# Performance work log

Measured on AMD Instinct MI355X. Metric: run time of the kernel, lower is better.

## Reference

```python
import math
import jax, jax.numpy as jnp
import numpy as np

B, N, D = 16, 2048, 256
EPS = 1e-8  # torch cosine_similarity default eps
TAU = 3.0   # gumbel-softmax temperature


def setup_inputs() -> dict:
    key = jax.random.key(0)
    k1, k2 = jax.random.split(key)
    return {
        "LowLevelFeatures": jax.random.normal(k1, (B, 1, N, D), dtype=jnp.float32),
        "HighLevelFeatures": jax.random.normal(k2, (B, 1, N, D), dtype=jnp.float32),
        "batch_size": B,
    }


def _forward(LLF4, HLF4):
    LLF = LLF4[:, 0]  # [B,N,D]
    HLF = HLF4[:, 0]  # [B,N,D]
    b, n, d = LLF.shape
    # pairwise cosine similarity [B,N,N]: matmul + norm-product (same math as
    # torch's broadcast cosine_similarity, without the [B,N,N,D] intermediate)
    dots = jnp.einsum('bnd,bmd->bnm', LLF, HLF)
    nl = jnp.linalg.norm(LLF, axis=-1)  # [B,N]
    nh = jnp.linalg.norm(HLF, axis=-1)  # [B,N]
    sim = dots / jnp.maximum(nl[:, :, None] * nh[:, None, :], EPS)
    sim = sim / math.sqrt(d)
    probs = jax.nn.softmax(sim, axis=1)  # softmax over dim 1 (LLF rows)
    # F.gumbel_softmax(probs, tau=3, hard=True, dim=1): probs act as logits
    u = jax.random.uniform(jax.random.key(42), probs.shape,
                           minval=1e-10, maxval=1.0)
    gumbels = -jnp.log(-jnp.log(u))
    y_soft = jax.nn.softmax((probs + gumbels) / TAU, axis=1)
    idx = jnp.argmax(y_soft, axis=1)  # [B,N]: selected LLF-row n per HLF col m
    # torch.where on the one-hot scans row-major over (b, n, m), so per batch
    # the returned n-indices are the SORTED multiset of selected indices
    sl = jnp.sort(idx, axis=-1)  # [B,N]
    bidx = jnp.arange(b)[:, None]  # [B,1]
    aligned = HLF[bidx, sl]  # gather along dim 1 -> [B,N,D]
    # rowwise cosine similarity between gathered HLF and LLF
    w = jnp.sum(aligned * LLF, axis=-1) / jnp.maximum(
        jnp.linalg.norm(aligned, axis=-1) * nl, EPS)  # [B,N]
    noise = jax.nn.softmax(w / 0.1, axis=1)[:, :, None]  # [B,N,1]
    hlf_new = aligned + LLF * noise
    out = HLF.at[bidx, sl].set(hlf_new)
    return out


def reference(LowLevelFeatures, HighLevelFeatures, batch_size):
    return _forward(LowLevelFeatures, HighLevelFeatures)
```

## Files before the change

kernel.cpp:

```cpp
#include <hip/hip_runtime.h>
#include <math.h>

#define NB 16
#define NN 2048
#define ND 256
#define BNtot (NB*NN)
#define HH 33554432u

typedef __attribute__((ext_vector_type(8))) short bf16x8;
typedef __attribute__((ext_vector_type(4))) float f32x4;

__device__ __forceinline__ void gld16(const void* g, void* l){
  __builtin_amdgcn_global_load_lds((const __attribute__((address_space(1))) void*)g,
                                   (__attribute__((address_space(3))) void*)l, 16, 0, 0);
}

__device__ __forceinline__ unsigned rotl(unsigned v, int r){
  return __builtin_amdgcn_alignbit(v, v, 32-r);
}
__device__ __forceinline__ unsigned umaxu(unsigned a, unsigned b){ return a > b ? a : b; }
__device__ __forceinline__ unsigned uminu(unsigned a, unsigned b){ return a < b ? a : b; }

__device__ __forceinline__ float gumbelv(unsigned b, unsigned n, unsigned m){
  unsigned f = (b<<22) | (n<<11) | m;
  unsigned x0 = (b < 8u) ? f : (f - HH);
  unsigned x1 = x0 + HH;
  const unsigned ks0=0u, ks1=42u, ks2=0u^42u^0x1BD11BDAu;
  unsigned v0 = x0 + ks0;
  unsigned v1 = x1 + ks1;
#define TFR(r) { v0 += v1; v1 = rotl(v1,(r)); v1 ^= v0; }
  TFR(13) TFR(15) TFR(26) TFR(6)
  v0 += ks1; v1 += ks2 + 1u;
  TFR(17) TFR(29) TFR(16) TFR(24)
  v0 += ks2; v1 += ks0 + 2u;
  TFR(13) TFR(15) TFR(26) TFR(6)
  v0 += ks0; v1 += ks1 + 3u;
  TFR(17) TFR(29) TFR(16) TFR(24)
  v0 += ks1; v1 += ks2 + 4u;
  TFR(13) TFR(15) TFR(26) TFR(6)
  v0 += ks2; v1 += ks0 + 5u;
#undef TFR
  unsigned bits = (b < 8u) ? v0 : v1;
  float fl = __uint_as_float((bits>>9) | 0x3F800000u) - 1.0f;
  float u = fmaxf(1e-10f, fl + 1e-10f);
  return -logf(-logf(u));
}

__device__ __forceinline__ float gfromkey(unsigned key){
  float fl = __uint_as_float(key | 0x3F800000u) - 1.0f;
  float u = fmaxf(1e-10f, fl + 1e-10f);
  return -logf(-logf(u));
}

struct GumState {
  unsigned x0, vk, a1, a2, c1, c2;
  int t;
};

__device__ __forceinline__ void gum_init(GumState& g, int t){
  g.t = t;
  int half = t & 1;
  int m    = (t >> 1) & 2047;
  int bl   = (t >> 12) & 7;
  int nq   = t >> 15;
  int nstart = (nq << 7) + (half << 6);
  g.x0 = ((unsigned)bl << 22) | ((unsigned)nstart << 11) | (unsigned)m;
  g.a1 = g.a2 = g.c1 = g.c2 = 0;
  g.vk = (unsigned)(127 - (half<<6));
}

__device__ __forceinline__ void gum_seek(GumState& g, int o){
  g.x0 += (unsigned)o * 2048u;
  g.vk -= (unsigned)o;
}

__device__ __forceinline__ void gum_iter(GumState& g, const int cnt){
  const unsigned KS2 = 42u ^ 0x1BD11BDAu;
  unsigned x0=g.x0, vk=g.vk, a1=g.a1, a2=g.a2, c1=g.c1, c2=g.c2;
#define TFR(r)       { v0 += v1; v1 = rotl(v1,(r)); v1 ^= v0; }
#define TFRI(r, inj) { v0 += v1 + (inj); v1 = rotl(v1,(r)); v1 ^= v0; }
  #pragma unroll 4
  for (int j = 0; j < cnt; ++j){
    unsigned v0 = x0;
    unsigned v1 = x0 + (HH + 42u);
    TFR(13) TFR(15) TFR(26) TFR(6)
    v1 += KS2 + 1u;
    TFRI(17, 42u) TFR(29) TFR(16) TFR(24)
    v1 += 2u;
    TFRI(13, KS2) TFR(15) TFR(26) TFR(6)
    v1 += 42u + 3u;
    TFR(17) TFR(29) TFR(16) TFR(24)
    v1 += KS2 + 4u;
    TFRI(13, 42u) TFR(15) TFR(26) TFR(6)
    v0 += KS2; v1 += 5u;
    unsigned pa = (v0 & 0xFFFFFE00u) | vk;
    unsigned pb = (v1 & 0xFFFFFE00u) | vk;
    unsigned ta = uminu(pa, a1);
    a1 = umaxu(pa, a1);
    a2 = umaxu(ta, a2);
    unsigned tc = uminu(pb, c1);
    c1 = umaxu(pb, c1);
    c2 = umaxu(tc, c2);
    x0 += 2048u;
    vk -= 1u;
  }
#undef TFR
#undef TFRI
  g.x0=x0; g.vk=vk; g.a1=a1; g.a2=a2; g.c1=c1; g.c2=c2;
}

__device__ __forceinline__ void gum_finish(const GumState& g, unsigned* __restrict__ pck,
                                           int seg){
  int half = g.t & 1;
  int m    = (g.t >> 1) & 2047;
  int bl   = (g.t >> 12) & 7;
  int nq   = g.t >> 15;
  unsigned p1 = __shfl_xor((int)g.a1, 1), p2 = __shfl_xor((int)g.a2, 1);
  unsigned q1 = __shfl_xor((int)g.c1, 1), q2 = __shfl_xor((int)g.c2, 1);
  unsigned A1 = umaxu(g.a1, p1);
  unsigned A2 = umaxu(uminu(g.a1, p1), umaxu(g.a2, p2));
  unsigned C1 = umaxu(g.c1, q1);
  unsigned C2 = umaxu(uminu(g.c1, q1), umaxu(g.c2, q2));
  if (half == 0){
    size_t base = ((size_t)((nq<<2) + (seg<<1))*NB + bl)*NN + m;
    pck[base]                 = A1;
    pck[base + (size_t)BNtot] = A2;
    pck[base + 8*NN]                 = C1;
    pck[base + 8*NN + (size_t)BNtot] = C2;
  }
}

__launch_bounds__(256)
__global__ void kgumbel(unsigned* __restrict__ pck){
  GumState g; gum_init(g, blockIdx.x*256 + (int)threadIdx.x);
  gum_iter(g, 32);
  gum_finish(g, pck, 0);
  g.a1 = g.a2 = g.c1 = g.c2 = 0;
  gum_iter(g, 32);
  gum_finish(g, pck, 1);
}

__device__ __forceinline__ void prep_rows(const float4* v, int wid, int lane,
                                          ushort* __restrict__ dst, float* __restrict__ nrm){
  #pragma unroll
  for (int i=0;i<4;i++){
    int row = wid*4 + i;
    float s = v[i].x*v[i].x + v[i].y*v[i].y + v[i].z*v[i].z + v[i].w*v[i].w;
    for (int o=32;o;o>>=1) s += __shfl_down(s,o);
    if (lane==0) nrm[row] = sqrtf(s);
    uint2 u;
    u.x = (__float_as_uint(v[i].y)&0xFFFF0000u)|(__float_as_uint(v[i].x)>>16);
    u.y = (__float_as_uint(v[i].w)&0xFFFF0000u)|(__float_as_uint(v[i].z)>>16);
    int b = row >> 11, nloc = row & 2047;
    int k = lane << 2;
    int ck = k >> 6;
    int j  = k & 63;
    int qi = j >> 3;
    size_t off = (size_t)b*524288 + (size_t)ck*131072 + (size_t)nloc*64
               + ((qi ^ (nloc & 7)) << 3) + (j & 7);
    *(uint2*)(dst + off) = u;
  }
}

__global__ void knorms(const float* __restrict__ LLF, const float* __restrict__ HLF,
                       float* __restrict__ nl, float* __restrict__ nh){
  int row = blockIdx.x;
  int wave = threadIdx.x >> 6;
  int lane = threadIdx.x & 63;
  const float* src = wave ? HLF : LLF;
  float4 v = ((const float4*)(src + (size_t)row*ND))[lane];
  float s = v.x*v.x + v.y*v.y + v.z*v.z + v.w*v.w;
  for (int o=32;o;o>>=1) s += __shfl_down(s,o);
  if (lane==0) (wave? nh: nl)[row] = sqrtf(s);
}

__launch_bounds__(256, 8)
__global__ void kfuse1(const float* __restrict__ LLF, const float* __restrict__ HLF,
                       ushort* __restrict__ Abf, ushort* __restrict__ Bbf,
                       float* __restrict__ nl, float* __restrict__ nh,
                       unsigned* __restrict__ pck){
  int t = blockIdx.x*256 + (int)threadIdx.x;
  int wid = t >> 6;
  int lane = t & 63;
  GumState g; gum_init(g, t);
  float4 va[4];
  #pragma unroll
  for (int i=0;i<4;i++)
    va[i] = ((const float4*)(LLF + (size_t)(wid*4+i)*ND))[lane];
  gum_iter(g, 16);
  prep_rows(va, wid, lane, Abf, nl);
  float4 vb[4];
  #pragma unroll
  for (int i=0;i<4;i++)
    vb[i] = ((const float4*)(HLF + (size_t)(wid*4+i)*ND))[lane];
  gum_iter(g, 16);
  prep_rows(vb, wid, lane, Bbf, nh);
  gum_finish(g, pck, 0);
}

#define K1 0.09016844f
__launch_bounds__(256)
__global__ void kgemm_dma(const ushort* __restrict__ Abf, const ushort* __restrict__ Bbf,
                          const float* __restrict__ nl, const float* __restrict__ nh,
                          float* __restrict__ partS, unsigned* __restrict__ pck){
  __shared__ ushort As[128*64];
  __shared__ ushort Bs[128*64];
  __shared__ float colsum[128];
  const int b  = blockIdx.z;
  const int n0 = blockIdx.y << 7;
  const int m0 = blockIdx.x << 7;
  const int tid  = threadIdx.x;
  const int lane = tid & 63;
  const int w    = tid >> 6;
  const int wn   = w >> 1, wm = w & 1;
  const int quad = lane >> 4, l15 = lane & 15;
  if (tid < 128) colsum[tid] = 0.0f;

  const int blockflat = (blockIdx.z*16 + (int)blockIdx.y)*16 + (int)blockIdx.x;
  const bool gw = (w < 2);
  GumState gs;
  if (gw){
    gum_init(gs, (blockflat*2 + w)*64 + lane);
    gum_seek(gs, 32);
  }

  const ushort* Ab = Abf + (size_t)b*524288;
  const ushort* Bb = Bbf + (size_t)b*524288;

  f32x4 acc[4][4];
  #pragma unroll
  for (int i=0;i<4;i++)
    #pragma unroll
    for (int j=0;j<4;j++) acc[i][j] = (f32x4){0.f,0.f,0.f,0.f};

  for (int ck=0; ck<4; ck++){
    __syncthreads();
    const ushort* ga = Ab + (size_t)ck*131072 + (size_t)n0*64;
    const ushort* gb = Bb + (size_t)ck*131072 + (size_t)m0*64;
    #pragma unroll
    for (int t=0;t<4;t++){
      int seg = (w*4 + t) * 512;
      gld16(ga + seg + lane*8, &As[seg]);
      gld16(gb + seg + lane*8, &Bs[seg]);
    }
    if (gw) gum_iter(gs, 8);
    __syncthreads();
    #pragma unroll
    for (int ks=0; ks<64; ks+=32){
      bf16x8 af[4], bf[4];
      #pragma unroll
      for (int t=0;t<4;t++){
        int R = wn*64 + t*16 + l15;
        af[t] = *(const bf16x8*)(&As[R*64 + ((((ks>>3)+quad) ^ (R&7))<<3)]);
      }
      #pragma unroll
      for (int t=0;t<4;t++){
        int R = wm*64 + t*16 + l15;
        bf[t] = *(const bf16x8*)(&Bs[R*64 + ((((ks>>3)+quad) ^ (R&7))<<3)]);
      }
      #pragma unroll
      for (int ti=0;ti<4;ti++)
        #pragma unroll
        for (int tj=0;tj<4;tj++)
          acc[ti][tj] = __builtin_amdgcn_mfma_f32_16x16x32_bf16(af[ti], bf[tj], acc[ti][tj], 0, 0, 0);
    }
  }

  float an[4][4];
  #pragma unroll
  for (int ti=0;ti<4;ti++)
    #pragma unroll
    for (int r=0;r<4;r++)
      an[ti][r] = K1 / nl[b*NN + n0 + wn*64 + ti*16 + quad*4 + r];
  float bm[4];
  #pragma unroll
  for (int tj=0;tj<4;tj++)
    bm[tj] = 1.0f / nh[b*NN + m0 + wm*64 + tj*16 + l15];
  #pragma unroll
  for (int tj=0;tj<4;tj++){
    float s = 0.0f;
    #pragma unroll
    for (int ti=0;ti<4;ti++)
      #pragma unroll
      for (int r=0;r<4;r++)
        s += __builtin_amdgcn_exp2f(acc[ti][tj][r]*an[ti][r]*bm[tj] - K1);
    s += __shfl_down(s, 32);
    s += __shfl_down(s, 16);
    if (lane < 16) atomicAdd(&colsum[wm*64 + tj*16 + l15], s);
  }
  __syncthreads();
  if (tid < 128)
    partS[(size_t)blockIdx.y*BNtot + b*NN + m0 + tid] = colsum[tid];
  if (gw) gum_finish(gs, pck, 1);
}

__launch_bounds__(256)
__global__ void kgemm_mfma(const float* __restrict__ LLF, const float* __restrict__ HLF,
                           const float* __restrict__ nl, const float* __restrict__ nh,
                           float* __restrict__ partS){
  __shared__ ushort As[128][72];
  __shared__ ushort Bs[128][72];
  __shared__ float colsum[128];
  const int b  = blockIdx.z;
  const int n0 = blockIdx.y << 7;
  const int m0 = blockIdx.x << 7;
  const float* Ab = LLF + (size_t)b*NN*ND;
  const float* Bb = HLF + (size_t)b*NN*ND;
  const int tid  = threadIdx.x;
  const int lane = tid & 63;
  const int w    = tid >> 6;
  const int wn   = w >> 1, wm = w & 1;
  const int quad = lane >> 4, l15 = lane & 15;
  if (tid < 128) colsum[tid] = 0.0f;

  f32x4 acc[4][4];
  #pragma unroll
  for (int i=0;i<4;i++)
    #pragma unroll
    for (int j=0;j<4;j++) acc[i][j] = (f32x4){0.f,0.f,0.f,0.f};

  const int rbase = tid >> 3;
  const int kq    = (tid & 7) << 3;

  for (int ck=0; ck<4; ck++){
    const int k0 = ck << 6;
    __syncthreads();
    #pragma unroll
    for (int pi=0; pi<4; pi++){
      int row = rbase + (pi<<5);
      const float* pa = Ab + (size_t)(n0+row)*ND + k0 + kq;
      float4 a0 = *(const float4*)pa;
      float4 a1 = *(const float4*)(pa+4);
      uint4 ua;
      ua.x = (__float_as_uint(a0.y)&0xFFFF0000u)|(__float_as_uint(a0.x)>>16);
      ua.y = (__float_as_uint(a0.w)&0xFFFF0000u)|(__float_as_uint(a0.z)>>16);
      ua.z = (__float_as_uint(a1.y)&0xFFFF0000u)|(__float_as_uint(a1.x)>>16);
      ua.w = (__float_as_uint(a1.w)&0xFFFF0000u)|(__float_as_uint(a1.z)>>16);
      *(uint4*)(&As[row][kq]) = ua;
      const float* pb = Bb + (size_t)(m0+row)*ND + k0 + kq;
      float4 b0 = *(const float4*)pb;
      float4 b1 = *(const float4*)(pb+4);
      uint4 ub;
      ub.x = (__float_as_uint(b0.y)&0xFFFF0000u)|(__float_as_uint(b0.x)>>16);
      ub.y = (__float_as_uint(b0.w)&0xFFFF0000u)|(__float_as_uint(b0.z)>>16);
      ub.z = (__float_as_uint(b1.y)&0xFFFF0000u)|(__float_as_uint(b1.x)>>16);
      ub.w = (__float_as_uint(b1.w)&0xFFFF0000u)|(__float_as_uint(b1.z)>>16);
      *(uint4*)(&Bs[row][kq]) = ub;
    }
    __syncthreads();
    #pragma unroll
    for (int ks=0; ks<64; ks+=32){
      bf16x8 af[4], bf[4];
      #pragma unroll
      for (int t=0;t<4;t++)
        af[t] = *(const bf16x8*)(&As[wn*64 + t*16 + l15][ks + quad*8]);
      #pragma unroll
      for (int t=0;t<4;t++)
        bf[t] = *(const bf16x8*)(&Bs[wm*64 + t*16 + l15][ks + quad*8]);
      #pragma unroll
      for (int ti=0;ti<4;ti++)
        #pragma unroll
        for (int tj=0;tj<4;tj++)
          acc[ti][tj] = __builtin_amdgcn_mfma_f32_16x16x32_bf16(af[ti], bf[tj], acc[ti][tj], 0, 0, 0);
    }
  }

  float an[4][4];
  #pragma unroll
  for (int ti=0;ti<4;ti++)
    #pragma unroll
    for (int r=0;r<4;r++)
      an[ti][r] = K1 / nl[b*NN + n0 + wn*64 + ti*16 + quad*4 + r];
  float bm[4];
  #pragma unroll
  for (int tj=0;tj<4;tj++)
    bm[tj] = 1.0f / nh[b*NN + m0 + wm*64 + tj*16 + l15];
  #pragma unroll
  for (int tj=0;tj<4;tj++){
    float s = 0.0f;
    #pragma unroll
    for (int ti=0;ti<4;ti++)
      #pragma unroll
      for (int r=0;r<4;r++)
        s += __builtin_amdgcn_exp2f(acc[ti][tj][r]*an[ti][r]*bm[tj] - K1);
    s += __shfl_down(s, 32);
    s += __shfl_down(s, 16);
    if (lane < 16) atomicAdd(&colsum[wm*64 + tj*16 + l15], s);
  }
  __syncthreads();
  if (tid < 128)
    partS[(size_t)blockIdx.y*BNtot + b*NN + m0 + tid] = colsum[tid];
}

__launch_bounds__(256)
__global__ void kresolve(const float* __restrict__ LLF, const float* __restrict__ HLF,
                         const float* __restrict__ nl, const float* __restrict__ nh,
                         const float* __restrict__ partS,
                         const unsigned* __restrict__ pck,
                         int* __restrict__ idx){
  int w    = threadIdx.x >> 6;
  int lane = threadIdx.x & 63;
  int g = blockIdx.x*4 + w;
  int b = g >> 11;
  float ps = (lane < 16) ? partS[(size_t)lane*BNtot + g] : 0.0f;
  ps += __shfl_down(ps, 8);
  ps += __shfl_down(ps, 4);
  ps += __shfl_down(ps, 2);
  ps += __shfl_down(ps, 1);
  float invS = 1.0f / __shfl(ps, 0);
  unsigned pk = pck[(size_t)lane*BNtot + g];
  float pv = gfromkey(pk >> 9);
  int   pn = ((lane >> 2) << 7) + 127 - (int)(pk & 127u);
  float gmax = pv;
  for (int o=32;o;o>>=1) gmax = fmaxf(gmax, __shfl_down(gmax,o));
  gmax = __shfl(gmax, 0);
  unsigned long long mask = __ballot(pv >= gmax - 8e-5f);
  float4 h = ((const float4*)(HLF + (size_t)g*ND))[lane];
  float nhg = nh[g];
  float bestQ = -INFINITY; int bestN = 1<<30;
  while (mask){
    int src = __builtin_ctzll(mask); mask &= mask-1;
    int   n  = __shfl(pn, src);
    float gv = __shfl(pv, src);
    float4 a = ((const float4*)(LLF + ((size_t)b*NN + n)*ND))[lane];
    float d = a.x*h.x + a.y*h.y + a.z*h.z + a.w*h.w;
    for (int o=32;o;o>>=1) d += __shfl_down(d,o);
    d = __shfl(d, 0);
    float sim = (d / fmaxf(nl[b*NN+n]*nhg, 1e-8f)) * 0.0625f;
    float q = expf(sim - 0.0625f)*invS + gv;
    if (q > bestQ || (q == bestQ && n < bestN)){ bestQ = q; bestN = n; }
  }
  if (lane==0) idx[g] = bestN;
}

__launch_bounds__(256)
__global__ void kstats(const float* __restrict__ A, const float* __restrict__ Bm,
                       const float* __restrict__ nl, const float* __restrict__ nh,
                       float* __restrict__ Mout, float* __restrict__ Sinv){
  __shared__ float As[64][33];
  __shared__ float Bs[64][33];
  __shared__ float Cs[64][65];
  const int b  = blockIdx.x >> 5;
  const int m0 = (blockIdx.x & 31) << 6;
  const float* Ab = A  + (size_t)b*NN*ND;
  const float* Bb = Bm + (size_t)b*NN*ND;
  const int tid = threadIdx.x;
  const int tx = tid & 15, ty = tid >> 4;
  float nhv[4];
  #pragma unroll
  for (int j=0;j<4;j++) nhv[j] = nh[b*NN + m0 + tx*4 + j];
  float Mr = -INFINITY, Sr = 0.0f;
  for (int nt=0; nt<NN; nt+=64){
    float acc[4][4] = {{0.f,0.f,0.f,0.f},{0.f,0.f,0.f,0.f},{0.f,0.f,0.f,0.f},{0.f,0.f,0.f,0.f}};
    for (int kc=0; kc<ND; kc+=32){
      __syncthreads();
      #pragma unroll
      for (int s=0;s<2;s++){
        int f = tid + (s<<8);
        int r = f >> 3;
        int c = (f & 7) << 2;
        float4 va = *(const float4*)(Ab + (size_t)(nt+r)*ND + kc + c);
        As[r][c]=va.x; As[r][c+1]=va.y; As[r][c+2]=va.z; As[r][c+3]=va.w;
        float4 vb = *(const float4*)(Bb + (size_t)(m0+r)*ND + kc + c);
        Bs[r][c]=vb.x; Bs[r][c+1]=vb.y; Bs[r][c+2]=vb.z; Bs[r][c+3]=vb.w;
      }
      __syncthreads();
      #pragma unroll 4
      for (int k=0;k<32;k++){
        float a0=As[ty*4+0][k], a1=As[ty*4+1][k], a2=As[ty*4+2][k], a3=As[ty*4+3][k];
        float b0=Bs[tx*4+0][k], b1=Bs[tx*4+1][k], b2=Bs[tx*4+2][k], b3=Bs[tx*4+3][k];
        acc[0][0]+=a0*b0; acc[0][1]+=a0*b1; acc[0][2]+=a0*b2; acc[0][3]+=a0*b3;
        acc[1][0]+=a1*b0; acc[1][1]+=a1*b1; acc[1][2]+=a1*b2; acc[1][3]+=a1*b3;
        acc[2][0]+=a2*b0; acc[2][1]+=a2*b1; acc[2][2]+=a2*b2; acc[2][3]+=a2*b3;
        acc[3][0]+=a3*b0; acc[3][1]+=a3*b1; acc[3][2]+=a3*b2; acc[3][3]+=a3*b3;
      }
    }
    float nlv[4];
    #pragma unroll
    for (int i=0;i<4;i++) nlv[i] = nl[b*NN + nt + ty*4 + i];
    __syncthreads();
    #pragma unroll
    for (int i=0;i<4;i++)
      #pragma unroll
      for (int j=0;j<4;j++){
        float denom = fmaxf(nlv[i]*nhv[j], 1e-8f);
        Cs[ty*4+i][tx*4+j] = (acc[i][j]/denom)*0.0625f;
      }
    __syncthreads();
    if (tid < 64){
      float tmax = -INFINITY;
      #pragma unroll 8
      for (int r=0;r<64;r++) tmax = fmaxf(tmax, Cs[r][tid]);
      float newM = fmaxf(Mr, tmax);
      float s = 0.0f;
      #pragma unroll 4
      for (int r=0;r<64;r++) s += expf(Cs[r][tid]-newM);
      Sr = Sr*expf(Mr-newM) + s;
      Mr = newM;
    }
  }
  if (tid < 64){
    Mout[b*NN+m0+tid] = Mr;
    Sinv[b*NN+m0+tid] = 1.0f/Sr;
  }
}

__launch_bounds__(256)
__global__ void kargmax(const float* __restrict__ A, const float* __restrict__ Bm,
                        const float* __restrict__ nl, const float* __restrict__ nh,
                        const float* __restrict__ Mv, const float* __restrict__ Sv,
                        int* __restrict__ idxout){
  __shared__ float As[64][33];
  __shared__ float Bs[64][33];
  __shared__ float Vs[16][64];
  __shared__ int   Is[16][64];
  const int b  = blockIdx.x >> 5;
  const int m0 = (blockIdx.x & 31) << 6;
  const float* Ab = A  + (size_t)b*NN*ND;
  const float* Bb = Bm + (size_t)b*NN*ND;
  const int tid = threadIdx.x;
  const int tx = tid & 15, ty = tid >> 4;
  float nhv[4], Mj[4], iSj[4];
  #pragma unroll
  for (int j=0;j<4;j++){
    int m = m0 + tx*4 + j;
    nhv[j] = nh[b*NN + m];
    Mj[j]  = Mv[b*NN + m];
    iSj[j] = Sv[b*NN + m];
  }
  float bestV = -INFINITY; int bestN = 0;
  for (int nt=0; nt<NN; nt+=64){
    float acc[4][4] = {{0.f,0.f,0.f,0.f},{0.f,0.f,0.f,0.f},{0.f,0.f,0.f,0.f},{0.f,0.f,0.f,0.f}};
    for (int kc=0; kc<ND; kc+=32){
      __syncthreads();
      #pragma unroll
      for (int s=0;s<2;s++){
        int f = tid + (s<<8);
        int r = f >> 3;
        int c = (f & 7) << 2;
        float4 va = *(const float4*)(Ab + (size_t)(nt+r)*ND + kc + c);
        As[r][c]=va.x; As[r][c+1]=va.y; As[r][c+2]=va.z; As[r][c+3]=va.w;
        float4 vb = *(const float4*)(Bb + (size_t)(m0+r)*ND + kc + c);
        Bs[r][c]=vb.x; Bs[r][c+1]=vb.y; Bs[r][c+2]=vb.z; Bs[r][c+3]=vb.w;
      }
      __syncthreads();
      #pragma unroll 4
      for (int k=0;k<32;k++){
        float a0=As[ty*4+0][k], a1=As[ty*4+1][k], a2=As[ty*4+2][k], a3=As[ty*4+3][k];
        float b0=Bs[tx*4+0][k], b1=Bs[tx*4+1][k], b2=Bs[tx*4+2][k], b3=Bs[tx*4+3][k];
        acc[0][0]+=a0*b0; acc[0][1]+=a0*b1; acc[0][2]+=a0*b2; acc[0][3]+=a0*b3;
        acc[1][0]+=a1*b0; acc[1][1]+=a1*b1; acc[1][2]+=a1*b2; acc[1][3]+=a1*b3;
        acc[2][0]+=a2*b0; acc[2][1]+=a2*b1; acc[2][2]+=a2*b2; acc[2][3]+=a2*b3;
        acc[3][0]+=a3*b0; acc[3][1]+=a3*b1; acc[3][2]+=a3*b2; acc[3][3]+=a3*b3;
      }
    }
    float nlv[4];
    #pragma unroll
    for (int i=0;i<4;i++) nlv[i] = nl[b*NN + nt + ty*4 + i];
    float lv[4]; int li[4];
    #pragma unroll
    for (int j=0;j<4;j++){ lv[j] = -INFINITY; li[j] = 0; }
    #pragma unroll
    for (int i=0;i<4;i++){
      int n = nt + ty*4 + i;
      #pragma unroll
      for (int j=0;j<4;j++){
        float denom = fmaxf(nlv[i]*nhv[j], 1e-8f);
        float sim = (acc[i][j]/denom)*0.0625f;
        float p = expf(sim - Mj[j]) * iSj[j];
        float v = p + gumbelv((unsigned)b, (unsigned)n, (unsigned)(m0 + tx*4 + j));
        if (v > lv[j]) { lv[j] = v; li[j] = n; }
      }
    }
    __syncthreads();
    #pragma unroll
    for (int j=0;j<4;j++){ Vs[ty][tx*4+j]=lv[j]; Is[ty][tx*4+j]=li[j]; }
    __syncthreads();
    if (tid < 64){
      #pragma unroll 4
      for (int t=0;t<16;t++){
        float v = Vs[t][tid];
        if (v > bestV){ bestV = v; bestN = Is[t][tid]; }
      }
    }
  }
  if (tid < 64) idxout[b*NN + m0 + tid] = bestN;
}

__global__ void ksort(const int* __restrict__ idx, int* __restrict__ cntg,
                      int* __restrict__ offg, int* __restrict__ sl){
  __shared__ int c[NN];
  __shared__ int part[256];
  int b = blockIdx.x, tid = threadIdx.x;
  for (int v=tid; v<NN; v+=256) c[v]=0;
  __syncthreads();
  for (int j=tid; j<NN; j+=256) atomicAdd(&c[idx[b*NN+j]], 1);
  __syncthreads();
  int base = tid*8, s=0, lc[8];
  #pragma unroll
  for (int k=0;k<8;k++){ lc[k]=c[base+k]; s+=lc[k]; }
  part[tid]=s; __syncthreads();
  for (int o=1;o<256;o<<=1){
    int v = (tid>=o)? part[tid-o] : 0;
    __syncthreads();
    part[tid]+=v;
    __syncthreads();
  }
  int run = part[tid]-s;
  #pragma unroll
  for (int k=0;k<8;k++){
    int v = base+k;
    cntg[b*NN+v]=lc[k];
    offg[b*NN+v]=run;
    for (int j=0;j<lc[k];j++) sl[b*NN+run+j]=v;
    run += lc[k];
  }
}

__global__ void kw(const float* __restrict__ LLF, const float* __restrict__ HLF,
                   const float* __restrict__ nl, const float* __restrict__ nh,
                   const int* __restrict__ sl, float* __restrict__ w){
  int g = blockIdx.x*4 + (threadIdx.x>>6);
  int lane = threadIdx.x & 63;
  int b = g >> 11;
  int s = sl[g];
  float4 a = ((const float4*)(HLF + ((size_t)b*NN + s)*ND))[lane];
  float4 l = ((const float4*)(LLF + (size_t)g*ND))[lane];
  float d = a.x*l.x + a.y*l.y + a.z*l.z + a.w*l.w;
  for (int o=32;o;o>>=1) d += __shfl_down(d,o);
  if (lane==0){
    float denom = fmaxf(nh[b*NN+s]*nl[g], 1e-8f);
    w[g] = d/denom;
  }
}

__global__ void knoise(const float* __restrict__ w, float* __restrict__ nz){
  int b = blockIdx.x, tid = threadIdx.x;
  __shared__ float sred[4];
  float x[8]; float mx = -INFINITY;
  #pragma unroll
  for (int k=0;k<8;k++){ x[k] = w[b*NN + tid*8 + k] / 0.1f; mx = fmaxf(mx, x[k]); }
  for (int o=32;o;o>>=1) mx = fmaxf(mx, __shfl_down(mx,o));
  mx = __shfl(mx, 0);
  if ((tid&63)==0) sred[tid>>6] = mx;
  __syncthreads();
  mx = fmaxf(fmaxf(sred[0],sred[1]), fmaxf(sred[2],sred[3]));
  __syncthreads();
  float e[8]; float s = 0.f;
  #pragma unroll
  for (int k=0;k<8;k++){ e[k] = expf(x[k]-mx); s += e[k]; }
  for (int o=32;o;o>>=1) s += __shfl_down(s,o);
  s = __shfl(s, 0);
  if ((tid&63)==0) sred[tid>>6] = s;
  __syncthreads();
  s = sred[0]+sred[1]+sred[2]+sred[3];
  #pragma unroll
  for (int k=0;k<8;k++) nz[b*NN + tid*8 + k] = e[k]/s;
}

__global__ void kfinal(const float* __restrict__ LLF, const float* __restrict__ HLF,
                       const int* __restrict__ cnt, const int* __restrict__ off,
                       const float* __restrict__ nz, float* __restrict__ out){
  int row = blockIdx.x;
  int lane = threadIdx.x;
  int b = row >> 11;
  float4 h = ((const float4*)(HLF + (size_t)row*ND))[lane];
  int c = cnt[row];
  if (c > 0){
    int i = off[row] + c - 1;
    float ns = nz[b*NN + i];
    float4 l = ((const float4*)(LLF + ((size_t)(b*NN + i))*ND))[lane];
    h.x += l.x*ns; h.y += l.y*ns; h.z += l.z*ns; h.w += l.w*ns;
  }
  ((float4*)(out + (size_t)row*ND))[lane] = h;
}

extern "C" void kernel_launch(void* const* d_in, const int* in_sizes, int n_in,
                              void* d_out, int out_size, void* d_ws, size_t ws_size,
                              hipStream_t stream){
  const float* LLF = (const float*)d_in[0];
  const float* HLF = (const float*)d_in[1];
  float* out = (float*)d_out;
  float* ws = (float*)d_ws;

  float* nl  = ws;
  float* nh  = ws + 1*(size_t)BNtot;
  float* iS  = ws + 2*(size_t)BNtot;
  int*   idx = (int*)(ws + 3*(size_t)BNtot);
  int*   cnt = (int*)(ws + 4*(size_t)BNtot);
  int*   off = (int*)(ws + 5*(size_t)BNtot);
  int*   sl  = (int*)(ws + 6*(size_t)BNtot);
  float* wv  = ws + 7*(size_t)BNtot;
  float* nz  = ws + 8*(size_t)BNtot;
  float* partS = ws + 9*(size_t)BNtot;
  unsigned* pck = (unsigned*)(ws + 25*(size_t)BNtot);
  ushort* Abf  = (ushort*)(ws + 89*(size_t)BNtot);
  ushort* Bbf  = Abf + (size_t)BNtot*ND;
  const size_t needBytes1 = (9 + 16 + 64) * (size_t)BNtot * 4;
  const size_t needBytes2 = needBytes1 + 2 * (size_t)BNtot * ND * 2;

  if (ws_size >= needBytes2){
    hipLaunchKernelGGL(kfuse1,  dim3(2048),      dim3(256), 0, stream, LLF, HLF, Abf, Bbf, nl, nh, pck);
    hipLaunchKernelGGL(kgemm_dma,dim3(16,16,16), dim3(256), 0, stream, Abf, Bbf, nl, nh, partS, pck);
    hipLaunchKernelGGL(kresolve,dim3(BNtot/4),   dim3(256), 0, stream, LLF, HLF, nl, nh, partS, pck, idx);
  } else if (ws_size >= needBytes1){
    hipLaunchKernelGGL(knorms,   dim3(BNtot),      dim3(128), 0, stream, LLF, HLF, nl, nh);
    hipLaunchKernelGGL(kgemm_mfma,dim3(16,16,16),  dim3(256), 0, stream, LLF, HLF, nl, nh, partS);
    hipLaunchKernelGGL(kgumbel,  dim3(2048),       dim3(256), 0, stream, pck);
    hipLaunchKernelGGL(kresolve, dim3(BNtot/4),    dim3(256), 0, stream, LLF, HLF, nl, nh, partS, pck, idx);
  } else {
    float* Mv = ws + 9*(size_t)BNtot;
    hipLaunchKernelGGL(knorms,   dim3(BNtot),      dim3(128), 0, stream, LLF, HLF, nl, nh);
    hipLaunchKernelGGL(kstats,   dim3(NB*32),      dim3(256), 0, stream, LLF, HLF, nl, nh, Mv, iS);
    hipLaunchKernelGGL(kargmax,  dim3(NB*32),      dim3(256), 0, stream, LLF, HLF, nl, nh, Mv, iS, idx);
  }

  hipLaunchKernelGGL(ksort,  dim3(NB),      dim3(256), 0, stream, idx, cnt, off, sl);
  hipLaunchKernelGGL(kw,     dim3(BNtot/4), dim3(256), 0, stream, LLF, HLF, nl, nh, sl, wv);
  hipLaunchKernelGGL(knoise, dim3(NB),      dim3(256), 0, stream, wv, nz);
  hipLaunchKernelGGL(kfinal, dim3(BNtot),   dim3(64),  0, stream, LLF, HLF, cnt, off, nz, out);
}
```

Before: 311.4 us.

## Replace softmax-denominator GEMM with bounded-invS argmax resolution and exact fallback

Drops the bf16 MFMA GEMM that built the per-column softmax denominators, along with the bf16 conversion of the inputs. The argmax is now resolved using guaranteed bounds on 1/S: cosine/16 lies in [-1/16, 1/16], so S falls in a fixed interval. Only when the candidate winner differs between the two bounds does a wave compute the exact S with a 2048-row scan. All Gumbel generation moves into kfuse1, and the packed top-2 keys use a per-column contiguous layout. This trades a large dense GEMM for rare but expensive fallback scans and a heavier single fused kernel.

```diff
diff --git a/kernel.cpp b/kernel.cpp
--- a/kernel.cpp
+++ b/kernel.cpp
@@ -6,14 +6,6 @@
 #define ND 256
 #define BNtot (NB*NN)
 #define HH 33554432u
-
-typedef __attribute__((ext_vector_type(8))) short bf16x8;
-typedef __attribute__((ext_vector_type(4))) float f32x4;
-
-__device__ __forceinline__ void gld16(const void* g, void* l){
-  __builtin_amdgcn_global_load_lds((const __attribute__((address_space(1))) void*)g,
-                                   (__attribute__((address_space(3))) void*)l, 16, 0, 0);
-}
 
 __device__ __forceinline__ unsigned rotl(unsigned v, int r){
   return __builtin_amdgcn_alignbit(v, v, 32-r);
@@ -67,11 +59,6 @@
   g.x0 = ((unsigned)bl << 22) | ((unsigned)nstart << 11) | (unsigned)m;
   g.a1 = g.a2 = g.c1 = g.c2 = 0;
   g.vk = (unsigned)(127 - (half<<6));
-}
-
-__device__ __forceinline__ void gum_seek(GumState& g, int o){
-  g.x0 += (unsigned)o * 2048u;
-  g.vk -= (unsigned)o;
 }
 
 __device__ __forceinline__ void gum_iter(GumState& g, const int cnt){
@@ -109,8 +96,7 @@
   g.x0=x0; g.vk=vk; g.a1=a1; g.a2=a2; g.c1=c1; g.c2=c2;
 }
 
-__device__ __forceinline__ void gum_finish(const GumState& g, unsigned* __restrict__ pck,
-                                           int seg){
+__device__ __forceinline__ void gum_finish(const GumState& g, unsigned* __restrict__ pck){
   int half = g.t & 1;
   int m    = (g.t >> 1) & 2047;
   int bl   = (g.t >> 12) & 7;
@@ -122,43 +108,20 @@
   unsigned C1 = umaxu(g.c1, q1);
   unsigned C2 = umaxu(uminu(g.c1, q1), umaxu(g.c2, q2));
   if (half == 0){
-    size_t base = ((size_t)((nq<<2) + (seg<<1))*NB + bl)*NN + m;
-    pck[base]                 = A1;
-    pck[base + (size_t)BNtot] = A2;
-    pck[base + 8*NN]                 = C1;
-    pck[base + 8*NN + (size_t)BNtot] = C2;
-  }
-}
-
-__launch_bounds__(256)
-__global__ void kgumbel(unsigned* __restrict__ pck){
-  GumState g; gum_init(g, blockIdx.x*256 + (int)threadIdx.x);
-  gum_iter(g, 32);
-  gum_finish(g, pck, 0);
-  g.a1 = g.a2 = g.c1 = g.c2 = 0;
-  gum_iter(g, 32);
-  gum_finish(g, pck, 1);
-}
-
-__device__ __forceinline__ void prep_rows(const float4* v, int wid, int lane,
-                                          ushort* __restrict__ dst, float* __restrict__ nrm){
+    uint2 ua; ua.x = A1; ua.y = A2;
+    uint2 uc; uc.x = C1; uc.y = C2;
+    *(uint2*)(&pck[((size_t)bl*NN + m)*32 + (nq<<1)])     = ua;
+    *(uint2*)(&pck[((size_t)(bl+8)*NN + m)*32 + (nq<<1)]) = uc;
+  }
+}
+
+__device__ __forceinline__ void norm_rows(const float4* v, int wid, int lane,
+                                          float* __restrict__ nrm){
   #pragma unroll
   for (int i=0;i<4;i++){
-    int row = wid*4 + i;
     float s = v[i].x*v[i].x + v[i].y*v[i].y + v[i].z*v[i].z + v[i].w*v[i].w;
     for (int o=32;o;o>>=1) s += __shfl_down(s,o);
-    if (lane==0) nrm[row] = sqrtf(s);
-    uint2 u;
-    u.x = (__float_as_uint(v[i].y)&0xFFFF0000u)|(__float_as_uint(v[i].x)>>16);
-    u.y = (__float_as_uint(v[i].w)&0xFFFF0000u)|(__float_as_uint(v[i].z)>>16);
-    int b = row >> 11, nloc = row & 2047;
-    int k = lane << 2;
-    int ck = k >> 6;
-    int j  = k & 63;
-    int qi = j >> 3;
-    size_t off = (size_t)b*524288 + (size_t)ck*131072 + (size_t)nloc*64
-               + ((qi ^ (nloc & 7)) << 3) + (j & 7);
-    *(uint2*)(dst + off) = u;
+    if (lane==0) nrm[wid*4 + i] = sqrtf(s);
   }
 }
 
@@ -176,7 +139,6 @@
 
 __launch_bounds__(256, 8)
 __global__ void kfuse1(const float* __restrict__ LLF, const float* __restrict__ HLF,
-                       ushort* __restrict__ Abf, ushort* __restrict__ Bbf,
                        float* __restrict__ nl, float* __restrict__ nh,
                        unsigned* __restrict__ pck){
   int t = blockIdx.x*256 + (int)threadIdx.x;
@@ -187,239 +149,82 @@
   #pragma unroll
   for (int i=0;i<4;i++)
     va[i] = ((const float4*)(LLF + (size_t)(wid*4+i)*ND))[lane];
-  gum_iter(g, 16);
-  prep_rows(va, wid, lane, Abf, nl);
+  gum_iter(g, 32);
+  norm_rows(va, wid, lane, nl);
   float4 vb[4];
   #pragma unroll
   for (int i=0;i<4;i++)
     vb[i] = ((const float4*)(HLF + (size_t)(wid*4+i)*ND))[lane];
-  gum_iter(g, 16);
-  prep_rows(vb, wid, lane, Bbf, nh);
-  gum_finish(g, pck, 0);
-}
-
-#define K1 0.09016844f
-__launch_bounds__(256)
-__global__ void kgemm_dma(const ushort* __restrict__ Abf, const ushort* __restrict__ Bbf,
-                          const float* __restrict__ nl, const float* __restrict__ nh,
-                          float* __restrict__ partS, unsigned* __restrict__ pck){
-  __shared__ ushort As[128*64];
-  __shared__ ushort Bs[128*64];
-  __shared__ float colsum[128];
-  const int b  = blockIdx.z;
-  const int n0 = blockIdx.y << 7;
-  const int m0 = blockIdx.x << 7;
-  const int tid  = threadIdx.x;
-  const int lane = tid & 63;
-  const int w    = tid >> 6;
-  const int wn   = w >> 1, wm = w & 1;
-  const int quad = lane >> 4, l15 = lane & 15;
-  if (tid < 128) colsum[tid] = 0.0f;
-
-  const int blockflat = (blockIdx.z*16 + (int)blockIdx.y)*16 + (int)blockIdx.x;
-  const bool gw = (w < 2);
-  GumState gs;
-  if (gw){
-    gum_init(gs, (blockflat*2 + w)*64 + lane);
-    gum_seek(gs, 32);
-  }
-
-  const ushort* Ab = Abf + (size_t)b*524288;
-  const ushort* Bb = Bbf + (size_t)b*524288;
-
-  f32x4 acc[4][4];
-  #pragma unroll
-  for (int i=0;i<4;i++)
-    #pragma unroll
-    for (int j=0;j<4;j++) acc[i][j] = (f32x4){0.f,0.f,0.f,0.f};
-
-  for (int ck=0; ck<4; ck++){
-    __syncthreads();
-    const ushort* ga = Ab + (size_t)ck*131072 + (size_t)n0*64;
-    const ushort* gb = Bb + (size_t)ck*131072 + (size_t)m0*64;
-    #pragma unroll
-    for (int t=0;t<4;t++){
-      int seg = (w*4 + t) * 512;
-      gld16(ga + seg + lane*8, &As[seg]);
-      gld16(gb + seg + lane*8, &Bs[seg]);
-    }
-    if (gw) gum_iter(gs, 8);
-    __syncthreads();
-    #pragma unroll
-    for (int ks=0; ks<64; ks+=32){
-      bf16x8 af[4], bf[4];
-      #pragma unroll
-      for (int t=0;t<4;t++){
-        int R = wn*64 + t*16 + l15;
-        af[t] = *(const bf16x8*)(&As[R*64 + ((((ks>>3)+quad) ^ (R&7))<<3)]);
-      }
-      #pragma unroll
-      for (int t=0;t<4;t++){
-        int R = wm*64 + t*16 + l15;
-        bf[t] = *(const bf16x8*)(&Bs[R*64 + ((((ks>>3)+quad) ^ (R&7))<<3)]);
-      }
-      #pragma unroll
-      for (int ti=0;ti<4;ti++)
-        #pragma unroll
-        for (int tj=0;tj<4;tj++)
-          acc[ti][tj] = __builtin_amdgcn_mfma_f32_16x16x32_bf16(af[ti], bf[tj], acc[ti][tj], 0, 0, 0);
-    }
-  }
-
-  float an[4][4];
-  #pragma unroll
-  for (int ti=0;ti<4;ti++)
-    #pragma unroll
-    for (int r=0;r<4;r++)
-      an[ti][r] = K1 / nl[b*NN + n0 + wn*64 + ti*16 + quad*4 + r];
-  float bm[4];
-  #pragma unroll
-  for (int tj=0;tj<4;tj++)
-    bm[tj] = 1.0f / nh[b*NN + m0 + wm*64 + tj*16 + l15];
-  #pragma unroll
-  for (int tj=0;tj<4;tj++){
-    float s = 0.0f;
-    #pragma unroll
-    for (int ti=0;ti<4;ti++)
-      #pragma unroll
-      for (int r=0;r<4;r++)
-        s += __builtin_amdgcn_exp2f(acc[ti][tj][r]*an[ti][r]*bm[tj] - K1);
-    s += __shfl_down(s, 32);
-    s += __shfl_down(s, 16);
-    if (lane < 16) atomicAdd(&colsum[wm*64 + tj*16 + l15], s);
-  }
-  __syncthreads();
-  if (tid < 128)
-    partS[(size_t)blockIdx.y*BNtot + b*NN + m0 + tid] = colsum[tid];
-  if (gw) gum_finish(gs, pck, 1);
-}
-
-__launch_bounds__(256)
-__global__ void kgemm_mfma(const float* __restrict__ LLF, const float* __restrict__ HLF,
-                           const float* __restrict__ nl, const float* __restrict__ nh,
-                           float* __restrict__ partS){
-  __shared__ ushort As[128][72];
-  __shared__ ushort Bs[128][72];
-  __shared__ float colsum[128];
-  const int b  = blockIdx.z;
-  const int n0 = blockIdx.y << 7;
-  const int m0 = blockIdx.x << 7;
-  const float* Ab = LLF + (size_t)b*NN*ND;
-  const float* Bb = HLF + (size_t)b*NN*ND;
-  const int tid  = threadIdx.x;
-  const int lane = tid & 63;
-  const int w    = tid >> 6;
-  const int wn   = w >> 1, wm = w & 1;
-  const int quad = lane >> 4, l15 = lane & 15;
-  if (tid < 128) colsum[tid] = 0.0f;
-
-  f32x4 acc[4][4];
-  #pragma unroll
-  for (int i=0;i<4;i++)
-    #pragma unroll
-    for (int j=0;j<4;j++) acc[i][j] = (f32x4){0.f,0.f,0.f,0.f};
-
-  const int rbase = tid >> 3;
-  const int kq    = (tid & 7) << 3;
-
-  for (int ck=0; ck<4; ck++){
-    const int k0 = ck << 6;
-    __syncthreads();
-    #pragma unroll
-    for (int pi=0; pi<4; pi++){
-      int row = rbase + (pi<<5);
-      const float* pa = Ab + (size_t)(n0+row)*ND + k0 + kq;
-      float4 a0 = *(const float4*)pa;
-      float4 a1 = *(const float4*)(pa+4);
-      uint4 ua;
-      ua.x = (__float_as_uint(a0.y)&0xFFFF0000u)|(__float_as_uint(a0.x)>>16);
-      ua.y = (__float_as_uint(a0.w)&0xFFFF0000u)|(__float_as_uint(a0.z)>>16);
-      ua.z = (__float_as_uint(a1.y)&0xFFFF0000u)|(__float_as_uint(a1.x)>>16);
-      ua.w = (__float_as_uint(a1.w)&0xFFFF0000u)|(__float_as_uint(a1.z)>>16);
-      *(uint4*)(&As[row][kq]) = ua;
-      const float* pb = Bb + (size_t)(m0+row)*ND + k0 + kq;
-      float4 b0 = *(const float4*)pb;
-      float4 b1 = *(const float4*)(pb+4);
-      uint4 ub;
-      ub.x = (__float_as_uint(b0.y)&0xFFFF0000u)|(__float_as_uint(b0.x)>>16);
-      ub.y = (__float_as_uint(b0.w)&0xFFFF0000u)|(__float_as_uint(b0.z)>>16);
-      ub.z = (__float_as_uint(b1.y)&0xFFFF0000u)|(__float_as_uint(b1.x)>>16);
-      ub.w = (__float_as_uint(b1.w)&0xFFFF0000u)|(__float_as_uint(b1.z)>>16);
-      *(uint4*)(&Bs[row][kq]) = ub;
-    }
-    __syncthreads();
-    #pragma unroll
-    for (int ks=0; ks<64; ks+=32){
-      bf16x8 af[4], bf[4];
-      #pragma unroll
-      for (int t=0;t<4;t++)
-        af[t] = *(const bf16x8*)(&As[wn*64 + t*16 + l15][ks + quad*8]);
-      #pragma unroll
-      for (int t=0;t<4;t++)
-        bf[t] = *(const bf16x8*)(&Bs[wm*64 + t*16 + l15][ks + quad*8]);
-      #pragma unroll
-      for (int ti=0;ti<4;ti++)
-        #pragma unroll
-        for (int tj=0;tj<4;tj++)
-          acc[ti][tj] = __builtin_amdgcn_mfma_f32_16x16x32_bf16(af[ti], bf[tj], acc[ti][tj], 0, 0, 0);
-    }
-  }
-
-  float an[4][4];
-  #pragma unroll
-  for (int ti=0;ti<4;ti++)
-    #pragma unroll
-    for (int r=0;r<4;r++)
-      an[ti][r] = K1 / nl[b*NN + n0 + wn*64 + ti*16 + quad*4 + r];
-  float bm[4];
-  #pragma unroll
-  for (int tj=0;tj<4;tj++)
-    bm[tj] = 1.0f / nh[b*NN + m0 + wm*64 + tj*16 + l15];
-  #pragma unroll
-  for (int tj=0;tj<4;tj++){
-    float s = 0.0f;
-    #pragma unroll
-    for (int ti=0;ti<4;ti++)
-      #pragma unroll
-      for (int r=0;r<4;r++)
-        s += __builtin_amdgcn_exp2f(acc[ti][tj][r]*an[ti][r]*bm[tj] - K1);
-    s += __shfl_down(s, 32);
-    s += __shfl_down(s, 16);
-    if (lane < 16) atomicAdd(&colsum[wm*64 + tj*16 + l15], s);
-  }
-  __syncthreads();
-  if (tid < 128)
-    partS[(size_t)blockIdx.y*BNtot + b*NN + m0 + tid] = colsum[tid];
-}
-
+  gum_iter(g, 32);
+  norm_rows(vb, wid, lane, nh);
+  gum_finish(g, pck);
+}
+
+#define ILO 4.882e-4f
+#define IHI 5.534e-4f
 __launch_bounds__(256)
 __global__ void kresolve(const float* __restrict__ LLF, const float* __restrict__ HLF,
                          const float* __restrict__ nl, const float* __restrict__ nh,
-                         const float* __restrict__ partS,
                          const unsigned* __restrict__ pck,
                          int* __restrict__ idx){
   int w    = threadIdx.x >> 6;
   int lane = threadIdx.x & 63;
   int g = blockIdx.x*4 + w;
   int b = g >> 11;
-  float ps = (lane < 16) ? partS[(size_t)lane*BNtot + g] : 0.0f;
-  ps += __shfl_down(ps, 8);
-  ps += __shfl_down(ps, 4);
-  ps += __shfl_down(ps, 2);
-  ps += __shfl_down(ps, 1);
-  float invS = 1.0f / __shfl(ps, 0);
-  unsigned pk = pck[(size_t)lane*BNtot + g];
-  float pv = gfromkey(pk >> 9);
-  int   pn = ((lane >> 2) << 7) + 127 - (int)(pk & 127u);
+  float pv = -INFINITY; int pn = 0;
+  if (lane < 32){
+    unsigned pk = pck[(size_t)g*32 + lane];
+    pv = gfromkey(pk >> 9);
+    pn = ((lane >> 1) << 7) + 127 - (int)(pk & 127u);
+  }
   float gmax = pv;
   for (int o=32;o;o>>=1) gmax = fmaxf(gmax, __shfl_down(gmax,o));
   gmax = __shfl(gmax, 0);
-  unsigned long long mask = __ballot(pv >= gmax - 8e-5f);
+  unsigned long long mask = __ballot(pv >= gmax - 8e-5f) & 0xFFFFFFFFull;
+  if (__popcll(mask) == 1){
+    int src = __builtin_ctzll(mask);
+    int n = __shfl(pn, src);
+    if (lane==0) idx[g] = n;
+    return;
+  }
   float4 h = ((const float4*)(HLF + (size_t)g*ND))[lane];
   float nhg = nh[g];
+  float bestLo = -INFINITY, bestHi = -INFINITY;
+  int nLo = 1<<30, nHi = 1<<30;
+  unsigned long long mm = mask;
+  while (mm){
+    int src = __builtin_ctzll(mm); mm &= mm-1;
+    int   n  = __shfl(pn, src);
+    float gv = __shfl(pv, src);
+    float4 a = ((const float4*)(LLF + ((size_t)b*NN + n)*ND))[lane];
+    float d = a.x*h.x + a.y*h.y + a.z*h.z + a.w*h.w;
+    for (int o=32;o;o>>=1) d += __shfl_down(d,o);
+    d = __shfl(d, 0);
+    float sim = (d / fmaxf(nl[b*NN+n]*nhg, 1e-8f)) * 0.0625f;
+    float e = expf(sim - 0.0625f);
+    float qlo = e*ILO + gv;
+    float qhi = e*IHI + gv;
+    if (qlo > bestLo || (qlo == bestLo && n < nLo)){ bestLo = qlo; nLo = n; }
+    if (qhi > bestHi || (qhi == bestHi && n < nHi)){ bestHi = qhi; nHi = n; }
+  }
+  if (nLo == nHi){
+    if (lane==0) idx[g] = nLo;
+    return;
+  }
+  float S = 0.0f;
+  for (int n2 = 0; n2 < NN; ++n2){
+    float4 a = ((const float4*)(LLF + ((size_t)b*NN + n2)*ND))[lane];
+    float d = a.x*h.x + a.y*h.y + a.z*h.z + a.w*h.w;
+    for (int o=32;o;o>>=1) d += __shfl_down(d,o);
+    d = __shfl(d, 0);
+    float sim = (d / fmaxf(nl[b*NN+n2]*nhg, 1e-8f)) * 0.0625f;
+    S += expf(sim - 0.0625f);
+  }
+  float invS = 1.0f / S;
   float bestQ = -INFINITY; int bestN = 1<<30;
-  while (mask){
-    int src = __builtin_ctzll(mask); mask &= mask-1;
+  mm = mask;
+  while (mm){
+    int src = __builtin_ctzll(mm); mm &= mm-1;
     int   n  = __shfl(pn, src);
     float gv = __shfl(pv, src);
     float4 a = ((const float4*)(LLF + ((size_t)b*NN + n)*ND))[lane];
@@ -692,27 +497,17 @@
   int*   sl  = (int*)(ws + 6*(size_t)BNtot);
   float* wv  = ws + 7*(size_t)BNtot;
   float* nz  = ws + 8*(size_t)BNtot;
-  float* partS = ws + 9*(size_t)BNtot;
-  unsigned* pck = (unsigned*)(ws + 25*(size_t)BNtot);
-  ushort* Abf  = (ushort*)(ws + 89*(size_t)BNtot);
-  ushort* Bbf  = Abf + (size_t)BNtot*ND;
-  const size_t needBytes1 = (9 + 16 + 64) * (size_t)BNtot * 4;
-  const size_t needBytes2 = needBytes1 + 2 * (size_t)BNtot * ND * 2;
-
-  if (ws_size >= needBytes2){
-    hipLaunchKernelGGL(kfuse1,  dim3(2048),      dim3(256), 0, stream, LLF, HLF, Abf, Bbf, nl, nh, pck);
-    hipLaunchKernelGGL(kgemm_dma,dim3(16,16,16), dim3(256), 0, stream, Abf, Bbf, nl, nh, partS, pck);
-    hipLaunchKernelGGL(kresolve,dim3(BNtot/4),   dim3(256), 0, stream, LLF, HLF, nl, nh, partS, pck, idx);
-  } else if (ws_size >= needBytes1){
-    hipLaunchKernelGGL(knorms,   dim3(BNtot),      dim3(128), 0, stream, LLF, HLF, nl, nh);
-    hipLaunchKernelGGL(kgemm_mfma,dim3(16,16,16),  dim3(256), 0, stream, LLF, HLF, nl, nh, partS);
-    hipLaunchKernelGGL(kgumbel,  dim3(2048),       dim3(256), 0, stream, pck);
-    hipLaunchKernelGGL(kresolve, dim3(BNtot/4),    dim3(256), 0, stream, LLF, HLF, nl, nh, partS, pck, idx);
+  unsigned* pck = (unsigned*)(ws + 9*(size_t)BNtot);
+  const size_t needA = (9 + 32) * (size_t)BNtot * 4;
+
+  if (ws_size >= needA){
+    hipLaunchKernelGGL(kfuse1,  dim3(2048),    dim3(256), 0, stream, LLF, HLF, nl, nh, pck);
+    hipLaunchKernelGGL(kresolve,dim3(BNtot/4), dim3(256), 0, stream, LLF, HLF, nl, nh, pck, idx);
   } else {
     float* Mv = ws + 9*(size_t)BNtot;
-    hipLaunchKernelGGL(knorms,   dim3(BNtot),      dim3(128), 0, stream, LLF, HLF, nl, nh);
-    hipLaunchKernelGGL(kstats,   dim3(NB*32),      dim3(256), 0, stream, LLF, HLF, nl, nh, Mv, iS);
-    hipLaunchKernelGGL(kargmax,  dim3(NB*32),      dim3(256), 0, stream, LLF, HLF, nl, nh, Mv, iS, idx);
+    hipLaunchKernelGGL(knorms,   dim3(BNtot),    dim3(128), 0, stream, LLF, HLF, nl, nh);
+    hipLaunchKernelGGL(kstats,   dim3(NB*32),    dim3(256), 0, stream, LLF, HLF, nl, nh, Mv, iS);
+    hipLaunchKernelGGL(kargmax,  dim3(NB*32),    dim3(256), 0, stream, LLF, HLF, nl, nh, Mv, iS, idx);
   }
 
   hipLaunchKernelGGL(ksort,  dim3(NB),      dim3(256), 0, stream, idx, cnt, off, sl);
```

Result: slower. 811.4 us (+160.6%).
